# Kernel tuning notes

Hardware: AMD Instinct MI355X
Metric: run time of the kernel (lower is better)

## Reference

```python
import jax, jax.numpy as jnp
import numpy as np

B, S, H = 8, 4096, 1152
LENGTH = 256


def setup_inputs() -> dict:
    key = jax.random.key(0)
    k1, k2 = jax.random.split(key)
    hidden_states = jax.random.normal(k1, (B, S, H), dtype=jnp.float32)
    # (x, y) patch coordinates on a 64x64 grid
    patch_positions = jax.random.randint(k2, (B, S, 2), 0, 64, dtype=jnp.int64)
    padding_positions = jnp.ones((B, LENGTH), dtype=jnp.bool_)
    return {
        "hidden_states": hidden_states,
        "patch_positions": patch_positions,
        "padding_positions": padding_positions,
    }


def _pool(hidden_states, patch_positions, length):
    b, s, h = hidden_states.shape
    k = int((s // length) ** 0.5)
    k_sq = k * k
    assert k_sq * length == s
    clamped = jnp.maximum(patch_positions, 0)  # clamp(min=0)
    max_x = jnp.max(clamped[..., 0], axis=-1, keepdims=True) + 1  # [B,1]
    kidx = clamped // k
    kernel_idxs = kidx[..., 0] + (max_x // k) * kidx[..., 1]  # [B,S], values < length
    # segment-mean instead of the one-hot GEMM: identical math
    seg = (kernel_idxs + length * jnp.arange(b, dtype=kernel_idxs.dtype)[:, None]).reshape(-1)
    pooled = jax.ops.segment_sum(
        hidden_states.reshape(b * s, h), seg, num_segments=b * length
    ).reshape(b, length, h) / k_sq
    counts = jax.ops.segment_sum(
        jnp.ones((b * s,), dtype=jnp.int32), seg, num_segments=b * length
    ).reshape(b, length)
    mask = counts > 0  # equivalent to ~(weights == 0).all(dim=1)
    return pooled, mask


def reference(hidden_states, patch_positions, padding_positions):
    length = LENGTH
    if hidden_states.shape[1] == length:
        pooled, mask = hidden_states, padding_positions
    else:
        pooled, mask = _pool(hidden_states, patch_positions, length)
    root_hidden_size = float(hidden_states.shape[-1]) ** 0.5
    pooled = pooled * root_hidden_size
    return pooled, mask
```

## Files before the change

kernel.cpp:

```cpp
#include <hip/hip_runtime.h>
#include <hip/hip_bf16.h>

#define NB 8
#define NS 4096
#define NH 1152
#define LEN 256
#define F4ROW (NH / 4)

__global__ void gvp_fused(const float* __restrict__ hidden,
                          const int* __restrict__ patch,
                          float* __restrict__ out,
                          float* __restrict__ maskout) {
    int g = blockIdx.x;
    int b = g >> 8;
    int myseg = g & (LEN - 1);
    int t = threadIdx.x;

    __shared__ int rows[NS];
    __shared__ int s_max[4];
    __shared__ int s_cnt;
    __shared__ int s_mult;
    if (t == 0) s_cnt = 0;

    const int2* p2 = (const int2*)(patch + (size_t)b * NS * 2);
    int pk[16];
    int m = 0;
    #pragma unroll
    for (int i = 0; i < 16; ++i) {
        int2 v = p2[t + 256 * i];
        int x = v.x < 0 ? 0 : v.x;
        int y = v.y < 0 ? 0 : v.y;
        pk[i] = x | (y << 16);
        m = max(m, x);
    }
    #pragma unroll
    for (int off = 32; off > 0; off >>= 1)
        m = max(m, __shfl_down(m, off, 64));
    if ((t & 63) == 0) s_max[t >> 6] = m;
    __syncthreads();
    if (t == 0)
        s_mult = (max(max(s_max[0], s_max[1]), max(s_max[2], s_max[3])) + 1) >> 2;
    __syncthreads();
    int mult = s_mult;

    #pragma unroll
    for (int i = 0; i < 16; ++i) {
        int x = pk[i] & 0xffff;
        int y = pk[i] >> 16;
        int seg = (x >> 2) + mult * (y >> 2);
        if (seg == myseg) {
            int pos = atomicAdd(&s_cnt, 1);
            rows[pos] = t + 256 * i;
        }
    }
    __syncthreads();
    int cnt = s_cnt;

    float4 a0 = make_float4(0.f, 0.f, 0.f, 0.f);
    float4 a1 = make_float4(0.f, 0.f, 0.f, 0.f);
    float4 c0 = make_float4(0.f, 0.f, 0.f, 0.f);
    float4 c1 = make_float4(0.f, 0.f, 0.f, 0.f);
    const float* hb = hidden + (size_t)b * NS * NH;
    int r = 0;
    for (; r + 3 < cnt; r += 4) {
        const float4* rA = (const float4*)(hb + (size_t)rows[r]     * NH);
        const float4* rB = (const float4*)(hb + (size_t)rows[r + 1] * NH);
        const float4* rC = (const float4*)(hb + (size_t)rows[r + 2] * NH);
        const float4* rD = (const float4*)(hb + (size_t)rows[r + 3] * NH);
        float4 vA = rA[t], vB = rB[t], vC = rC[t], vD = rD[t];
        a0.x += vA.x + vB.x; a0.y += vA.y + vB.y; a0.z += vA.z + vB.z; a0.w += vA.w + vB.w;
        c0.x += vC.x + vD.x; c0.y += vC.y + vD.y; c0.z += vC.z + vD.z; c0.w += vC.w + vD.w;
        if (t < F4ROW - 256) {
            float4 wA = rA[t + 256], wB = rB[t + 256], wC = rC[t + 256], wD = rD[t + 256];
            a1.x += wA.x + wB.x; a1.y += wA.y + wB.y; a1.z += wA.z + wB.z; a1.w += wA.w + wB.w;
            c1.x += wC.x + wD.x; c1.y += wC.y + wD.y; c1.z += wC.z + wD.z; c1.w += wC.w + wD.w;
        }
    }
    for (; r < cnt; ++r) {
        const float4* rA = (const float4*)(hb + (size_t)rows[r] * NH);
        float4 vA = rA[t];
        a0.x += vA.x; a0.y += vA.y; a0.z += vA.z; a0.w += vA.w;
        if (t < F4ROW - 256) {
            float4 wA = rA[t + 256];
            a1.x += wA.x; a1.y += wA.y; a1.z += wA.z; a1.w += wA.w;
        }
    }
    a0.x += c0.x; a0.y += c0.y; a0.z += c0.z; a0.w += c0.w;
    a1.x += c1.x; a1.y += c1.y; a1.z += c1.z; a1.w += c1.w;

    const float scale = 2.1213203435596424f;
    float4* og = (float4*)(out + (size_t)g * NH);
    og[t] = make_float4(a0.x * scale, a0.y * scale, a0.z * scale, a0.w * scale);
    if (t < F4ROW - 256)
        og[t + 256] = make_float4(a1.x * scale, a1.y * scale, a1.z * scale, a1.w * scale);
    if (t == 0) maskout[g] = (cnt > 0) ? 1.0f : 0.0f;
}

extern "C" void kernel_launch(void* const* d_in, const int* in_sizes, int n_in,
                              void* d_out, int out_size, void* d_ws, size_t ws_size,
                              hipStream_t stream) {
    const float* hidden = (const float*)d_in[0];
    const int*   patch  = (const int*)d_in[1];
    float* out = (float*)d_out;
    float* maskout = out + (size_t)NB * LEN * NH;

    gvp_fused<<<NB * LEN, 256, 0, stream>>>(hidden, patch, out, maskout);
}
```

Measured before the change: 31.86 us.

## Spread row tail columns across all threads and unroll gather by eight

Each row is 288 float4 wide and there are 256 threads. Previously only 32 threads handled the tail 32 float4s, so seven of eight waves sat idle during those loads. Now all 256 threads cover the first 256 float4s, and the tail columns are split so that 8 groups of 32 threads each sum every eighth row. Those partial sums are reduced through shared memory, reusing the rows buffer. The main loop is also unrolled to 8 rows per iteration using native vector types, which adds more loads in flight at the cost of an extra barrier and a shared-memory reduction.

```diff
diff --git a/kernel.cpp b/kernel.cpp
--- a/kernel.cpp
+++ b/kernel.cpp
@@ -7,16 +7,19 @@
 #define LEN 256
 #define F4ROW (NH / 4)
 
-__global__ void gvp_fused(const float* __restrict__ hidden,
-                          const int* __restrict__ patch,
-                          float* __restrict__ out,
-                          float* __restrict__ maskout) {
+typedef float vf4 __attribute__((ext_vector_type(4)));
+
+__global__ __launch_bounds__(256) void gvp_fused(
+        const float* __restrict__ hidden,
+        const int* __restrict__ patch,
+        float* __restrict__ out,
+        float* __restrict__ maskout) {
     int g = blockIdx.x;
     int b = g >> 8;
     int myseg = g & (LEN - 1);
     int t = threadIdx.x;
 
-    __shared__ int rows[NS];
+    __shared__ __align__(16) int rows[NS];
     __shared__ int s_max[4];
     __shared__ int s_cnt;
     __shared__ int s_mult;
@@ -56,43 +59,51 @@
     __syncthreads();
     int cnt = s_cnt;
 
-    float4 a0 = make_float4(0.f, 0.f, 0.f, 0.f);
-    float4 a1 = make_float4(0.f, 0.f, 0.f, 0.f);
-    float4 c0 = make_float4(0.f, 0.f, 0.f, 0.f);
-    float4 c1 = make_float4(0.f, 0.f, 0.f, 0.f);
     const float* hb = hidden + (size_t)b * NS * NH;
+    vf4 a0 = 0.f, a1 = 0.f;
     int r = 0;
-    for (; r + 3 < cnt; r += 4) {
-        const float4* rA = (const float4*)(hb + (size_t)rows[r]     * NH);
-        const float4* rB = (const float4*)(hb + (size_t)rows[r + 1] * NH);
-        const float4* rC = (const float4*)(hb + (size_t)rows[r + 2] * NH);
-        const float4* rD = (const float4*)(hb + (size_t)rows[r + 3] * NH);
-        float4 vA = rA[t], vB = rB[t], vC = rC[t], vD = rD[t];
-        a0.x += vA.x + vB.x; a0.y += vA.y + vB.y; a0.z += vA.z + vB.z; a0.w += vA.w + vB.w;
-        c0.x += vC.x + vD.x; c0.y += vC.y + vD.y; c0.z += vC.z + vD.z; c0.w += vC.w + vD.w;
-        if (t < F4ROW - 256) {
-            float4 wA = rA[t + 256], wB = rB[t + 256], wC = rC[t + 256], wD = rD[t + 256];
-            a1.x += wA.x + wB.x; a1.y += wA.y + wB.y; a1.z += wA.z + wB.z; a1.w += wA.w + wB.w;
-            c1.x += wC.x + wD.x; c1.y += wC.y + wD.y; c1.z += wC.z + wD.z; c1.w += wC.w + wD.w;
-        }
+    for (; r + 7 < cnt; r += 8) {
+        const vf4* p0 = (const vf4*)(hb + (size_t)rows[r + 0] * NH);
+        const vf4* p1 = (const vf4*)(hb + (size_t)rows[r + 1] * NH);
+        const vf4* p2r = (const vf4*)(hb + (size_t)rows[r + 2] * NH);
+        const vf4* p3 = (const vf4*)(hb + (size_t)rows[r + 3] * NH);
+        const vf4* p4 = (const vf4*)(hb + (size_t)rows[r + 4] * NH);
+        const vf4* p5 = (const vf4*)(hb + (size_t)rows[r + 5] * NH);
+        const vf4* p6 = (const vf4*)(hb + (size_t)rows[r + 6] * NH);
+        const vf4* p7 = (const vf4*)(hb + (size_t)rows[r + 7] * NH);
+        vf4 v0 = p0[t], v1 = p1[t], v2 = p2r[t], v3 = p3[t];
+        vf4 v4 = p4[t], v5 = p5[t], v6 = p6[t], v7 = p7[t];
+        v0 += v1; v2 += v3; v4 += v5; v6 += v7;
+        v0 += v2; v4 += v6;
+        a0 += v0; a1 += v4;
     }
     for (; r < cnt; ++r) {
-        const float4* rA = (const float4*)(hb + (size_t)rows[r] * NH);
-        float4 vA = rA[t];
-        a0.x += vA.x; a0.y += vA.y; a0.z += vA.z; a0.w += vA.w;
-        if (t < F4ROW - 256) {
-            float4 wA = rA[t + 256];
-            a1.x += wA.x; a1.y += wA.y; a1.z += wA.z; a1.w += wA.w;
-        }
+        const vf4* p0 = (const vf4*)(hb + (size_t)rows[r] * NH);
+        a0 += p0[t];
     }
-    a0.x += c0.x; a0.y += c0.y; a0.z += c0.z; a0.w += c0.w;
-    a1.x += c1.x; a1.y += c1.y; a1.z += c1.z; a1.w += c1.w;
+    a0 += a1;
+
+    int l = t & 31;
+    int grp = t >> 5;
+    vf4 a2 = 0.f;
+    for (int r2 = grp; r2 < cnt; r2 += 8) {
+        const vf4* p = (const vf4*)(hb + (size_t)rows[r2] * NH);
+        a2 += p[256 + l];
+    }
+    __syncthreads();
+    vf4* red = (vf4*)rows;
+    red[t] = a2;
+    __syncthreads();
 
     const float scale = 2.1213203435596424f;
-    float4* og = (float4*)(out + (size_t)g * NH);
-    og[t] = make_float4(a0.x * scale, a0.y * scale, a0.z * scale, a0.w * scale);
-    if (t < F4ROW - 256)
-        og[t + 256] = make_float4(a1.x * scale, a1.y * scale, a1.z * scale, a1.w * scale);
+    vf4* og = (vf4*)(out + (size_t)g * NH);
+    og[t] = a0 * scale;
+    if (t < 32) {
+        vf4 s = 0.f;
+        #pragma unroll
+        for (int j = 0; j < 8; ++j) s += red[j * 32 + t];
+        og[256 + t] = s * scale;
+    }
     if (t == 0) maskout[g] = (cnt > 0) ? 1.0f : 0.0f;
 }
 
```

Result: no change. 31.94 us (+0.2%).
